# Performance work log

Hardware: AMD Instinct MI355X
Metric: run time of the kernel (lower is better)

## Reference

```python
import jax, jax.numpy as jnp
import numpy as np

N, IN_DIM, OUT_DIM, NUM_EXPERTS, TOP_K = 8192, 1024, 1024, 8, 2


def setup_inputs() -> dict:
    key = jax.random.key(0)
    ks = jax.random.split(key, 5)
    s_in = 1.0 / np.sqrt(IN_DIM)
    x = jax.random.normal(ks[0], (N, IN_DIM), dtype=jnp.float32)
    # per-expert Linear weights: [E, in, out] (torch Linear weight is [out,in]; we store transposed)
    W = jax.random.uniform(ks[1], (NUM_EXPERTS, IN_DIM, OUT_DIM), jnp.float32, -s_in, s_in)
    b = jax.random.uniform(ks[2], (NUM_EXPERTS, OUT_DIM), jnp.float32, -s_in, s_in)
    Wg = jax.random.uniform(ks[3], (IN_DIM, NUM_EXPERTS), jnp.float32, -s_in, s_in)
    bg = jax.random.uniform(ks[4], (NUM_EXPERTS,), jnp.float32, -s_in, s_in)
    return {"x": x, "W": W, "b": b, "Wg": Wg, "bg": bg}


def reference(x, W, b, Wg, bg):
    # gating scores [N, E]
    scores = x @ Wg + bg
    # top-k mask
    _, top_idx = jax.lax.top_k(scores, TOP_K)  # [N, k]
    mask = jnp.zeros_like(scores).at[jnp.arange(x.shape[0])[:, None], top_idx].set(1.0)
    masked = jnp.where(mask == 0, -jnp.inf, scores)
    gating_weights = jax.nn.softmax(masked, axis=-1)  # [N, E]
    # all-expert linear: [N, E, out]
    expert_outputs = jnp.einsum('ni,eio->neo', x, W) + b
    # weighted combine over experts
    return jnp.einsum('ne,neo->no', gating_weights, expert_outputs)
```

## Files before the change

### kernel.cpp

```cpp
#include <hip/hip_runtime.h>

#define N_TOK 8192
#define IN_DIM 1024
#define OUT_DIM 1024
#define NE 8
#define TILE_SH 12288

typedef short short8 __attribute__((ext_vector_type(8)));
typedef float f32x4 __attribute__((ext_vector_type(4)));
typedef ushort ushort4v __attribute__((ext_vector_type(4)));

__device__ __forceinline__ ushort f2bf(float f) {
    union { float f; unsigned u; } v; v.f = f;
    unsigned u = v.u;
    unsigned r = (u + 0x7fffu + ((u >> 16) & 1u)) >> 16;
    return (ushort)r;
}

__device__ __forceinline__ float bf2f(short s) {
    union { unsigned u; float f; } v;
    v.u = ((unsigned)(unsigned short)s) << 16;
    return v.f;
}

__device__ __forceinline__ void gl_lds16(const short* g, short* l) {
    __builtin_amdgcn_global_load_lds(
        (const __attribute__((address_space(1))) unsigned int*)g,
        (__attribute__((address_space(3))) unsigned int*)l, 16, 0, 0);
}

__global__ __launch_bounds__(256) void prep(const float* __restrict__ x,
                                            const float* __restrict__ Wg,
                                            const float* __restrict__ bg,
                                            const float* __restrict__ W,
                                            short* __restrict__ xb,
                                            short* __restrict__ wt,
                                            unsigned* __restrict__ choice,
                                            float2* __restrict__ wts) {
    __shared__ ushort tile[32][33];
    int bid = blockIdx.x;
    if (bid < 2048) {
        int wid = threadIdx.x >> 6, lane = threadIdx.x & 63;
        int tok = bid * 4 + wid;
        const float* xr = x + (size_t)tok * IN_DIM;
        short* xbr = xb + (size_t)tok * IN_DIM;
        float acc[8];
        #pragma unroll
        for (int e = 0; e < 8; ++e) acc[e] = 0.f;
        #pragma unroll
        for (int it = 0; it < 4; ++it) {
            int j = it * 256 + lane * 4;
            float4 v = *(const float4*)(xr + j);
            ushort4v o;
            o[0] = f2bf(v.x); o[1] = f2bf(v.y); o[2] = f2bf(v.z); o[3] = f2bf(v.w);
            *(ushort4v*)(xbr + j) = o;
            #pragma unroll
            for (int r = 0; r < 4; ++r) {
                float xv = (r == 0) ? v.x : (r == 1) ? v.y : (r == 2) ? v.z : v.w;
                float4 wa = *(const float4*)(Wg + (size_t)(j + r) * 8);
                float4 wb = *(const float4*)(Wg + (size_t)(j + r) * 8 + 4);
                acc[0] += xv * wa.x; acc[1] += xv * wa.y;
                acc[2] += xv * wa.z; acc[3] += xv * wa.w;
                acc[4] += xv * wb.x; acc[5] += xv * wb.y;
                acc[6] += xv * wb.z; acc[7] += xv * wb.w;
            }
        }
        #pragma unroll
        for (int e = 0; e < 8; ++e)
            #pragma unroll
            for (int off = 32; off; off >>= 1)
                acc[e] += __shfl_xor(acc[e], off, 64);
        if (lane == 0) {
            float s[8];
            #pragma unroll
            for (int e = 0; e < 8; ++e) s[e] = acc[e] + bg[e];
            int i0 = 0;
            #pragma unroll
            for (int e = 1; e < 8; ++e) if (s[e] > s[i0]) i0 = e;
            int i1 = (i0 == 0) ? 1 : 0;
            #pragma unroll
            for (int e = 0; e < 8; ++e) if (e != i0 && s[e] > s[i1]) i1 = e;
            float e0 = 1.f, e1 = __expf(s[i1] - s[i0]);
            float inv = 1.f / (e0 + e1);
            choice[tok] = (unsigned)i0 | ((unsigned)i1 << 8);
            wts[tok] = make_float2(e0 * inv, e1 * inv);
        }
    } else {
        int id = bid - 2048;
        int nt = id & 31, kt = (id >> 5) & 31, e = id >> 10;
        int t = threadIdx.x;
        int r = t >> 3;
        int c4 = (t & 7) * 4;
        const float4 v = *(const float4*)(W + (((size_t)e * 1024 + kt * 32 + r) * 1024) + nt * 32 + c4);
        tile[c4 + 0][r] = f2bf(v.x);
        tile[c4 + 1][r] = f2bf(v.y);
        tile[c4 + 2][r] = f2bf(v.z);
        tile[c4 + 3][r] = f2bf(v.w);
        __syncthreads();
        int n = t >> 3, kq = (t & 7) * 4;
        ushort4v o;
        o[0] = tile[n][kq + 0]; o[1] = tile[n][kq + 1];
        o[2] = tile[n][kq + 2]; o[3] = tile[n][kq + 3];
        *(ushort4v*)(wt + (((size_t)e * 1024 + nt * 32 + n) * 1024) + kt * 32 + kq) = o;
    }
}

__global__ __launch_bounds__(1024) void bucket(const unsigned* __restrict__ choice,
                                               int* __restrict__ counts,
                                               int* __restrict__ entries,
                                               int* __restrict__ inv0,
                                               int* __restrict__ inv1) {
    int e = blockIdx.x;
    int t = threadIdx.x;
    int wid = t >> 6, lane = t & 63;
    __shared__ int wsum[16];
    unsigned c[8];
    #pragma unroll
    for (int chunk = 0; chunk < 8; ++chunk) c[chunk] = choice[chunk * 1024 + t];
    int base = 0;
    #pragma unroll
    for (int chunk = 0; chunk < 8; ++chunk) {
        int tok = chunk * 1024 + t;
        int which = ((int)(c[chunk] & 255u) == e) ? 0
                  : (((int)((c[chunk] >> 8) & 255u) == e) ? 1 : -1);
        unsigned long long m = __ballot(which >= 0);
        if (lane == 0) wsum[wid] = __popcll(m);
        __syncthreads();
        int woff = base;
        #pragma unroll
        for (int i = 0; i < 16; ++i) if (i < wid) woff += wsum[i];
        int tot = 0;
        #pragma unroll
        for (int i = 0; i < 16; ++i) tot += wsum[i];
        if (which >= 0) {
            int rank = __popcll(m & ((1ull << lane) - 1ull));
            int idx = woff + rank;
            entries[e * N_TOK + idx] = tok;
            if (which == 0) inv0[tok] = idx; else inv1[tok] = idx;
        }
        base += tot;
        __syncthreads();
    }
    if (t == 0) counts[e] = base;
}

__global__ __launch_bounds__(256, 2) void moe_gemm(const short* __restrict__ xb,
                                                   const short* __restrict__ wt,
                                                   const float* __restrict__ bias,
                                                   const int* __restrict__ counts,
                                                   const int* __restrict__ entries,
                                                   short* __restrict__ ys) {
    int lin = blockIdx.x;
    int e = lin & 7;
    int inner = lin >> 3;
    int ct = inner & 3, rt = inner >> 2;
    int cnt = counts[e];
    if (rt * 128 >= cnt) return;
    int rows = min(128, cnt - rt * 128);
    int base_e = 0;
    #pragma unroll
    for (int i = 0; i < NE; ++i) base_e += (i < e) ? counts[i] : 0;

    __shared__ __align__(16) short lds[3 * TILE_SH];
    __shared__ int tok_sh[128];

    int t = threadIdx.x, wid = t >> 6, lane = t & 63;
    int ebase = e * N_TOK + rt * 128;
    if (t < 128) tok_sh[t] = (t < rows) ? entries[ebase + t] : entries[ebase];
    __syncthreads();

    int chunkoff = (((t & 3) ^ ((t >> 2) & 3)) * 8);
    const short* asrc0 = xb + (size_t)tok_sh[t >> 2] * IN_DIM + chunkoff;
    const short* asrc1 = xb + (size_t)tok_sh[64 + (t >> 2)] * IN_DIM + chunkoff;
    const short* bsrc0 = wt + ((size_t)e * OUT_DIM + ct * 256 + (t >> 2)) * IN_DIM + chunkoff;
    const short* bsrc1 = bsrc0 + (size_t)64 * IN_DIM;
    const short* bsrc2 = bsrc0 + (size_t)128 * IN_DIM;
    const short* bsrc3 = bsrc0 + (size_t)192 * IN_DIM;
    int dst8 = t * 8;

    int wr = wid >> 1, wc = wid & 1;
    int frow = lane & 15, fslot = lane >> 4;
    int rslot = (fslot ^ (frow & 3)) * 8;
    int aoff[4], boff[8];
    #pragma unroll
    for (int mi = 0; mi < 4; ++mi) aoff[mi] = (wr * 64 + mi * 16 + frow) * 32 + rslot;
    #pragma unroll
    for (int ni = 0; ni < 8; ++ni) boff[ni] = (wc * 128 + ni * 16 + frow) * 32 + rslot;

    f32x4 acc[4][8];
    #pragma unroll
    for (int mi = 0; mi < 4; ++mi)
        #pragma unroll
        for (int ni = 0; ni < 8; ++ni) acc[mi][ni] = (f32x4)(0.0f);

#define STAGE(BUF, KT)                                                        \
    {                                                                         \
        short* nb = lds + (BUF) * TILE_SH;                                    \
        int nk = (KT) * 32;                                                   \
        gl_lds16(asrc0 + nk, nb + dst8);                                      \
        gl_lds16(asrc1 + nk, nb + 2048 + dst8);                               \
        gl_lds16(bsrc0 + nk, nb + 4096 + dst8);                               \
        gl_lds16(bsrc1 + nk, nb + 6144 + dst8);                               \
        gl_lds16(bsrc2 + nk, nb + 8192 + dst8);                               \
        gl_lds16(bsrc3 + nk, nb + 10240 + dst8);                              \
    }

#define GITER(CUR, NXT, KTN, VN, DO_STAGE)                                    \
    {                                                                         \
        asm volatile("s_waitcnt vmcnt(" VN ")" ::: "memory");                 \
        __builtin_amdgcn_s_barrier();                                         \
        __builtin_amdgcn_sched_barrier(0);                                    \
        const short* Ab = lds + (CUR) * TILE_SH;                              \
        const short* Bb = Ab + 4096;                                          \
        short8 afv[4], bfv[8];                                                \
        _Pragma("unroll")                                                     \
        for (int mi = 0; mi < 4; ++mi) afv[mi] = *(const short8*)(Ab + aoff[mi]); \
        _Pragma("unroll")                                                     \
        for (int ni = 0; ni < 8; ++ni) bfv[ni] = *(const short8*)(Bb + boff[ni]); \
        if (DO_STAGE) STAGE(NXT, KTN);                                        \
        __builtin_amdgcn_s_setprio(1);                                        \
        _Pragma("unroll")                                                     \
        for (int mi = 0; mi < 4; ++mi)                                        \
            _Pragma("unroll")                                                 \
            for (int ni = 0; ni < 8; ++ni)                                    \
                acc[mi][ni] = __builtin_amdgcn_mfma_f32_16x16x32_bf16(        \
                    afv[mi], bfv[ni], acc[mi][ni], 0, 0, 0);                  \
        __builtin_amdgcn_s_setprio(0);                                        \
    }

    STAGE(0, 0);
    STAGE(1, 1);

    for (int kt = 0; kt < 30; kt += 3) {
        GITER(0, 2, kt + 2, "6", 1);
        GITER(1, 0, kt + 3, "6", 1);
        GITER(2, 1, kt + 4, "6", 1);
    }
    GITER(0, 0, 0, "6", 0);
    GITER(1, 0, 0, "0", 0);

#undef GITER
#undef STAGE

    __syncthreads();
    short* ep = lds;
    const float* be = bias + (size_t)e * OUT_DIM;
    #pragma unroll
    for (int ni = 0; ni < 8; ++ni) {
        int col = wc * 128 + ni * 16 + frow;
        float bv = be[ct * 256 + col];
        #pragma unroll
        for (int mi = 0; mi < 4; ++mi) {
            int rb_ = wr * 64 + mi * 16 + fslot * 4;
            #pragma unroll
            for (int r = 0; r < 4; ++r)
                ep[(rb_ + r) * 268 + col] = (short)f2bf(acc[mi][ni][r] + bv);
        }
    }
    __syncthreads();
    #pragma unroll
    for (int k = 0; k < 16; ++k) {
        int f = t + k * 256;
        int row = f >> 5, cw = f & 31;
        if (row < rows) {
            short8 v = *(const short8*)(ep + row * 268 + cw * 8);
            *(short8*)(ys + ((size_t)(base_e + rt * 128 + row)) * OUT_DIM
                       + ct * 256 + cw * 8) = v;
        }
    }
}

__global__ __launch_bounds__(256) void combine(const short* __restrict__ ys,
                                               const unsigned* __restrict__ choice,
                                               const float2* __restrict__ wts,
                                               const int* __restrict__ inv0,
                                               const int* __restrict__ inv1,
                                               const int* __restrict__ counts,
                                               float* __restrict__ out) {
    __shared__ int bases[8];
    if (threadIdx.x < 8) {
        int s = 0;
        #pragma unroll
        for (int i = 0; i < 8; ++i) s += (i < (int)threadIdx.x) ? counts[i] : 0;
        bases[threadIdx.x] = s;
    }
    __syncthreads();
    int tok = blockIdx.x * 2 + (threadIdx.x >> 7);
    int c8 = (threadIdx.x & 127) * 8;
    unsigned ch = choice[tok];
    float2 w = wts[tok];
    int p0 = bases[ch & 255u] + inv0[tok];
    int p1 = bases[(ch >> 8) & 255u] + inv1[tok];
    short8 a = *(const short8*)(ys + (size_t)p0 * OUT_DIM + c8);
    short8 b = *(const short8*)(ys + (size_t)p1 * OUT_DIM + c8);
    float* op = out + (size_t)tok * OUT_DIM + c8;
    float4 o0, o1;
    o0.x = w.x * bf2f(a[0]) + w.y * bf2f(b[0]);
    o0.y = w.x * bf2f(a[1]) + w.y * bf2f(b[1]);
    o0.z = w.x * bf2f(a[2]) + w.y * bf2f(b[2]);
    o0.w = w.x * bf2f(a[3]) + w.y * bf2f(b[3]);
    o1.x = w.x * bf2f(a[4]) + w.y * bf2f(b[4]);
    o1.y = w.x * bf2f(a[5]) + w.y * bf2f(b[5]);
    o1.z = w.x * bf2f(a[6]) + w.y * bf2f(b[6]);
    o1.w = w.x * bf2f(a[7]) + w.y * bf2f(b[7]);
    *(float4*)op = o0;
    *(float4*)(op + 4) = o1;
}

extern "C" void kernel_launch(void* const* d_in, const int* in_sizes, int n_in,
                              void* d_out, int out_size, void* d_ws, size_t ws_size,
                              hipStream_t stream) {
    const float* x  = (const float*)d_in[0];
    const float* W  = (const float*)d_in[1];
    const float* b  = (const float*)d_in[2];
    const float* Wg = (const float*)d_in[3];
    const float* bg = (const float*)d_in[4];
    float* out = (float*)d_out;

    char* ws = (char*)d_ws;
    short* xb        = (short*)(ws);
    short* wt        = (short*)(ws + 16777216);
    unsigned* choice = (unsigned*)(ws + 33554432);
    float2* wts      = (float2*)(ws + 33587200);
    int* inv0        = (int*)(ws + 33652736);
    int* inv1        = (int*)(ws + 33685504);
    int* entries     = (int*)(ws + 33718272);
    int* counts      = (int*)(ws + 34242560);
    short* ys        = (short*)(ws + 34242624);

    prep<<<10240, 256, 0, stream>>>(x, Wg, bg, W, xb, wt, choice, wts);
    bucket<<<8, 1024, 0, stream>>>(choice, counts, entries, inv0, inv1);
    moe_gemm<<<2048, 256, 0, stream>>>(xb, wt, b, counts, entries, ys);
    combine<<<4096, 256, 0, stream>>>(ys, choice, wts, inv0, inv1, counts, out);
}
```

Baseline: 115.7 us.

## Prefetch LDS fragments for next k-tile after MFMA block in GEMM loop

Restructures the main loop so that LDS fragment reads for the next k-tile happen at the end of each iteration, after waiting for the global-to-LDS copy and a barrier. The next stage's global loads are issued before the MFMA block. The aim is to take the LDS read latency out of the stretch between the barrier and the MFMAs and to overlap global staging with compute. In exchange it adds a second barrier per iteration and a different wait placement, which could add synchronization stalls or race on buffer reuse.

```diff
diff --git a/kernel.cpp b/kernel.cpp
--- a/kernel.cpp
+++ b/kernel.cpp
@@ -193,6 +193,8 @@
         #pragma unroll
         for (int ni = 0; ni < 8; ++ni) acc[mi][ni] = (f32x4)(0.0f);
 
+    short8 caf[4], cbf[8];
+
 #define STAGE(BUF, KT)                                                        \
     {                                                                         \
         short* nb = lds + (BUF) * TILE_SH;                                    \
@@ -205,41 +207,50 @@
         gl_lds16(bsrc3 + nk, nb + 10240 + dst8);                              \
     }
 
-#define GITER(CUR, NXT, KTN, VN, DO_STAGE)                                    \
+#define LOADFRAGS(BUF)                                                        \
     {                                                                         \
-        asm volatile("s_waitcnt vmcnt(" VN ")" ::: "memory");                 \
+        const short* Ab = lds + (BUF) * TILE_SH;                              \
+        const short* Bb = Ab + 4096;                                          \
+        _Pragma("unroll")                                                     \
+        for (int mi = 0; mi < 4; ++mi) caf[mi] = *(const short8*)(Ab + aoff[mi]); \
+        _Pragma("unroll")                                                     \
+        for (int ni = 0; ni < 8; ++ni) cbf[ni] = *(const short8*)(Bb + boff[ni]); \
+        __builtin_amdgcn_sched_barrier(0);                                    \
+    }
+
+#define GITER(NXTBUF, STGBUF, KTN, VN, DO_STAGE, DO_TAIL)                     \
+    {                                                                         \
+        if (DO_STAGE) STAGE(STGBUF, KTN);                                     \
         __builtin_amdgcn_s_barrier();                                         \
-        __builtin_amdgcn_sched_barrier(0);                                    \
-        const short* Ab = lds + (CUR) * TILE_SH;                              \
-        const short* Bb = Ab + 4096;                                          \
-        short8 afv[4], bfv[8];                                                \
-        _Pragma("unroll")                                                     \
-        for (int mi = 0; mi < 4; ++mi) afv[mi] = *(const short8*)(Ab + aoff[mi]); \
-        _Pragma("unroll")                                                     \
-        for (int ni = 0; ni < 8; ++ni) bfv[ni] = *(const short8*)(Bb + boff[ni]); \
-        if (DO_STAGE) STAGE(NXT, KTN);                                        \
         __builtin_amdgcn_s_setprio(1);                                        \
         _Pragma("unroll")                                                     \
         for (int mi = 0; mi < 4; ++mi)                                        \
             _Pragma("unroll")                                                 \
             for (int ni = 0; ni < 8; ++ni)                                    \
                 acc[mi][ni] = __builtin_amdgcn_mfma_f32_16x16x32_bf16(        \
-                    afv[mi], bfv[ni], acc[mi][ni], 0, 0, 0);                  \
+                    caf[mi], cbf[ni], acc[mi][ni], 0, 0, 0);                  \
         __builtin_amdgcn_s_setprio(0);                                        \
+        asm volatile("s_waitcnt vmcnt(" VN ")" ::: "memory");                 \
+        __builtin_amdgcn_s_barrier();                                         \
+        if (DO_TAIL) LOADFRAGS(NXTBUF);                                       \
     }
 
     STAGE(0, 0);
     STAGE(1, 1);
+    asm volatile("s_waitcnt vmcnt(6)" ::: "memory");
+    __builtin_amdgcn_s_barrier();
+    LOADFRAGS(0);
 
     for (int kt = 0; kt < 30; kt += 3) {
-        GITER(0, 2, kt + 2, "6", 1);
-        GITER(1, 0, kt + 3, "6", 1);
-        GITER(2, 1, kt + 4, "6", 1);
-    }
-    GITER(0, 0, 0, "6", 0);
-    GITER(1, 0, 0, "0", 0);
+        GITER(1, 2, kt + 2, "6", 1, 1);
+        GITER(2, 0, kt + 3, "6", 1, 1);
+        GITER(0, 1, kt + 4, "6", 1, 1);
+    }
+    GITER(1, 0, 0, "0", 0, 1);
+    GITER(0, 0, 0, "0", 0, 0);
 
 #undef GITER
+#undef LOADFRAGS
 #undef STAGE
 
     __syncthreads();
```

Measured after the change: 113.2 us. -2.2%, faster.

## Restructure MoE GEMM to 8 waves, BK=64 double buffer with fragment prefetch

Applied to the files above, without the earlier changes.

The grouped expert GEMM moves from 4 waves to 8 waves per block, so each wave owns a 64x64 output sub-tile instead of 64x128. The K step grows from 32 to 64 with an 8-chunk XOR swizzle, and the pipeline changes from a three-stage buffer to a two-stage one. The first half of the next tile's fragments is prefetched from LDS after the barrier. This halves the number of barrier iterations and raises wave-level parallelism to hide latency. In exchange it waits on vmcnt(0) every iteration, so global loads have less lead time, and register and LDS use per block changes.

```diff
diff --git a/kernel.cpp b/kernel.cpp
--- a/kernel.cpp
+++ b/kernel.cpp
@@ -4,7 +4,7 @@
 #define IN_DIM 1024
 #define OUT_DIM 1024
 #define NE 8
-#define TILE_SH 12288
+#define TSH 24576
 
 typedef short short8 __attribute__((ext_vector_type(8)));
 typedef float f32x4 __attribute__((ext_vector_type(4)));
@@ -144,7 +144,7 @@
     if (t == 0) counts[e] = base;
 }
 
-__global__ __launch_bounds__(256, 2) void moe_gemm(const short* __restrict__ xb,
+__global__ __launch_bounds__(512, 2) void moe_gemm(const short* __restrict__ xb,
                                                    const short* __restrict__ wt,
                                                    const float* __restrict__ bias,
                                                    const int* __restrict__ counts,
@@ -161,7 +161,7 @@
     #pragma unroll
     for (int i = 0; i < NE; ++i) base_e += (i < e) ? counts[i] : 0;
 
-    __shared__ __align__(16) short lds[3 * TILE_SH];
+    __shared__ __align__(16) short lds[2 * TSH];
     __shared__ int tok_sh[128];
 
     int t = threadIdx.x, wid = t >> 6, lane = t & 63;
@@ -169,85 +169,114 @@
     if (t < 128) tok_sh[t] = (t < rows) ? entries[ebase + t] : entries[ebase];
     __syncthreads();
 
-    int chunkoff = (((t & 3) ^ ((t >> 2) & 3)) * 8);
-    const short* asrc0 = xb + (size_t)tok_sh[t >> 2] * IN_DIM + chunkoff;
-    const short* asrc1 = xb + (size_t)tok_sh[64 + (t >> 2)] * IN_DIM + chunkoff;
-    const short* bsrc0 = wt + ((size_t)e * OUT_DIM + ct * 256 + (t >> 2)) * IN_DIM + chunkoff;
+    int r0 = t >> 3;
+    int chunkoff = (((t & 7) ^ (r0 & 7)) * 8);
+    const short* asrc0 = xb + (size_t)tok_sh[r0] * IN_DIM + chunkoff;
+    const short* asrc1 = xb + (size_t)tok_sh[64 + r0] * IN_DIM + chunkoff;
+    const short* bsrc0 = wt + ((size_t)e * OUT_DIM + ct * 256 + r0) * IN_DIM + chunkoff;
     const short* bsrc1 = bsrc0 + (size_t)64 * IN_DIM;
     const short* bsrc2 = bsrc0 + (size_t)128 * IN_DIM;
     const short* bsrc3 = bsrc0 + (size_t)192 * IN_DIM;
     int dst8 = t * 8;
 
-    int wr = wid >> 1, wc = wid & 1;
+    int wr = wid >> 2, wc = wid & 3;
     int frow = lane & 15, fslot = lane >> 4;
-    int rslot = (fslot ^ (frow & 3)) * 8;
-    int aoff[4], boff[8];
-    #pragma unroll
-    for (int mi = 0; mi < 4; ++mi) aoff[mi] = (wr * 64 + mi * 16 + frow) * 32 + rslot;
-    #pragma unroll
-    for (int ni = 0; ni < 8; ++ni) boff[ni] = (wc * 128 + ni * 16 + frow) * 32 + rslot;
-
-    f32x4 acc[4][8];
+    int aoff[2][4], boff[2][4];
+    #pragma unroll
+    for (int mi = 0; mi < 4; ++mi) {
+        int ra = wr * 64 + mi * 16 + frow;
+        #pragma unroll
+        for (int kk = 0; kk < 2; ++kk)
+            aoff[kk][mi] = ra * 64 + (((kk * 4 + fslot) ^ (ra & 7)) * 8);
+    }
+    #pragma unroll
+    for (int ni = 0; ni < 4; ++ni) {
+        int rb = wc * 64 + ni * 16 + frow;
+        #pragma unroll
+        for (int kk = 0; kk < 2; ++kk)
+            boff[kk][ni] = 8192 + rb * 64 + (((kk * 4 + fslot) ^ (rb & 7)) * 8);
+    }
+
+    f32x4 acc[4][4];
     #pragma unroll
     for (int mi = 0; mi < 4; ++mi)
         #pragma unroll
-        for (int ni = 0; ni < 8; ++ni) acc[mi][ni] = (f32x4)(0.0f);
+        for (int ni = 0; ni < 4; ++ni) acc[mi][ni] = (f32x4)(0.0f);
+
+    short8 caf[4], cbf[4];
 
 #define STAGE(BUF, KT)                                                        \
     {                                                                         \
-        short* nb = lds + (BUF) * TILE_SH;                                    \
-        int nk = (KT) * 32;                                                   \
+        short* nb = lds + (BUF) * TSH;                                        \
+        int nk = (KT) * 64;                                                   \
         gl_lds16(asrc0 + nk, nb + dst8);                                      \
-        gl_lds16(asrc1 + nk, nb + 2048 + dst8);                               \
-        gl_lds16(bsrc0 + nk, nb + 4096 + dst8);                               \
-        gl_lds16(bsrc1 + nk, nb + 6144 + dst8);                               \
-        gl_lds16(bsrc2 + nk, nb + 8192 + dst8);                               \
-        gl_lds16(bsrc3 + nk, nb + 10240 + dst8);                              \
-    }
-
-#define GITER(CUR, NXT, KTN, VN, DO_STAGE)                                    \
+        gl_lds16(asrc1 + nk, nb + 4096 + dst8);                               \
+        gl_lds16(bsrc0 + nk, nb + 8192 + dst8);                               \
+        gl_lds16(bsrc1 + nk, nb + 12288 + dst8);                              \
+        gl_lds16(bsrc2 + nk, nb + 16384 + dst8);                              \
+        gl_lds16(bsrc3 + nk, nb + 20480 + dst8);                              \
+    }
+
+#define LOADKK0(BUF)                                                          \
     {                                                                         \
-        asm volatile("s_waitcnt vmcnt(" VN ")" ::: "memory");                 \
-        __builtin_amdgcn_s_barrier();                                         \
+        const short* Ab = lds + (BUF) * TSH;                                  \
+        _Pragma("unroll")                                                     \
+        for (int mi = 0; mi < 4; ++mi) caf[mi] = *(const short8*)(Ab + aoff[0][mi]); \
+        _Pragma("unroll")                                                     \
+        for (int ni = 0; ni < 4; ++ni) cbf[ni] = *(const short8*)(Ab + boff[0][ni]); \
         __builtin_amdgcn_sched_barrier(0);                                    \
-        const short* Ab = lds + (CUR) * TILE_SH;                              \
-        const short* Bb = Ab + 4096;                                          \
-        short8 afv[4], bfv[8];                                                \
-        _Pragma("unroll")                                                     \
-        for (int mi = 0; mi < 4; ++mi) afv[mi] = *(const short8*)(Ab + aoff[mi]); \
-        _Pragma("unroll")                                                     \
-        for (int ni = 0; ni < 8; ++ni) bfv[ni] = *(const short8*)(Bb + boff[ni]); \
+    }
+
+#define GITER(CUR, NXT, KTN, DO_STAGE, DO_TAIL)                               \
+    {                                                                         \
         if (DO_STAGE) STAGE(NXT, KTN);                                        \
+        const short* Ab = lds + (CUR) * TSH;                                  \
+        short8 af1[4], bf1[4];                                                \
+        _Pragma("unroll")                                                     \
+        for (int mi = 0; mi < 4; ++mi) af1[mi] = *(const short8*)(Ab + aoff[1][mi]); \
+        _Pragma("unroll")                                                     \
+        for (int ni = 0; ni < 4; ++ni) bf1[ni] = *(const short8*)(Ab + boff[1][ni]); \
         __builtin_amdgcn_s_setprio(1);                                        \
         _Pragma("unroll")                                                     \
         for (int mi = 0; mi < 4; ++mi)                                        \
             _Pragma("unroll")                                                 \
-            for (int ni = 0; ni < 8; ++ni)                                    \
+            for (int ni = 0; ni < 4; ++ni)                                    \
                 acc[mi][ni] = __builtin_amdgcn_mfma_f32_16x16x32_bf16(        \
-                    afv[mi], bfv[ni], acc[mi][ni], 0, 0, 0);                  \
+                    caf[mi], cbf[ni], acc[mi][ni], 0, 0, 0);                  \
+        _Pragma("unroll")                                                     \
+        for (int mi = 0; mi < 4; ++mi)                                        \
+            _Pragma("unroll")                                                 \
+            for (int ni = 0; ni < 4; ++ni)                                    \
+                acc[mi][ni] = __builtin_amdgcn_mfma_f32_16x16x32_bf16(        \
+                    af1[mi], bf1[ni], acc[mi][ni], 0, 0, 0);                  \
         __builtin_amdgcn_s_setprio(0);                                        \
+        asm volatile("s_waitcnt vmcnt(0)" ::: "memory");                      \
+        __builtin_amdgcn_s_barrier();                                         \
+        if (DO_TAIL) LOADKK0(NXT);                                            \
     }
 
     STAGE(0, 0);
-    STAGE(1, 1);
-
-    for (int kt = 0; kt < 30; kt += 3) {
-        GITER(0, 2, kt + 2, "6", 1);
-        GITER(1, 0, kt + 3, "6", 1);
-        GITER(2, 1, kt + 4, "6", 1);
-    }
-    GITER(0, 0, 0, "6", 0);
-    GITER(1, 0, 0, "0", 0);
+    asm volatile("s_waitcnt vmcnt(0)" ::: "memory");
+    __builtin_amdgcn_s_barrier();
+    LOADKK0(0);
+
+    for (int kt2 = 0; kt2 < 7; ++kt2) {
+        GITER(0, 1, 2 * kt2 + 1, 1, 1);
+        GITER(1, 0, 2 * kt2 + 2, 1, 1);
+    }
+    GITER(0, 1, 15, 1, 1);
+    GITER(1, 0, 0, 0, 0);
 
 #undef GITER
+#undef LOADKK0
 #undef STAGE
 
     __syncthreads();
     short* ep = lds;
     const float* be = bias + (size_t)e * OUT_DIM;
     #pragma unroll
-    for (int ni = 0; ni < 8; ++ni) {
-        int col = wc * 128 + ni * 16 + frow;
+    for (int ni = 0; ni < 4; ++ni) {
+        int col = wc * 64 + ni * 16 + frow;
         float bv = be[ct * 256 + col];
         #pragma unroll
         for (int mi = 0; mi < 4; ++mi) {
@@ -259,8 +288,8 @@
     }
     __syncthreads();
     #pragma unroll
-    for (int k = 0; k < 16; ++k) {
-        int f = t + k * 256;
+    for (int k = 0; k < 8; ++k) {
+        int f = t + k * 512;
         int row = f >> 5, cw = f & 31;
         if (row < rows) {
             short8 v = *(const short8*)(ep + row * 268 + cw * 8);
@@ -330,6 +359,6 @@
 
     prep<<<10240, 256, 0, stream>>>(x, Wg, bg, W, xb, wt, choice, wts);
     bucket<<<8, 1024, 0, stream>>>(choice, counts, entries, inv0, inv1);
-    moe_gemm<<<2048, 256, 0, stream>>>(xb, wt, b, counts, entries, ys);
+    moe_gemm<<<2048, 512, 0, stream>>>(xb, wt, b, counts, entries, ys);
     combine<<<4096, 256, 0, stream>>>(ys, choice, wts, inv0, inv1, counts, out);
 }
```

Measured after the change: 119.3 us. +3.1%, slower.
